# Performance work log

Hardware: AMD Instinct MI355X
Metric: run time of the kernel (lower is better)

Reference implementation:

```python
import jax, jax.numpy as jnp
import numpy as np

B, P = 64, 256          # graphs, nodes per graph
N = B * P
IN, H, C, OUT = 4096, 512, 12, 5
E0 = 131072             # directed edges before symmetrization
EPS = 1e-15


def setup_inputs() -> dict:
    key = jax.random.key(0)
    ks = jax.random.split(key, 12)
    x = jax.random.normal(ks[0], (N, IN), jnp.float32)
    # within-graph random edges, then symmetrize (to_undirected)
    src0 = jax.random.randint(ks[1], (E0,), 0, N)
    off = jax.random.randint(ks[2], (E0,), 0, P)
    dst0 = (src0 // P) * P + off
    edge_index = jnp.stack([jnp.concatenate([src0, dst0]),
                            jnp.concatenate([dst0, src0])])
    batch = jnp.repeat(jnp.arange(B, dtype=jnp.int32), P)
    p = lambda k, sh: 0.02 * jax.random.normal(k, sh, jnp.float32)
    return dict(
        x=x, edge_index=edge_index, batch=batch,
        W1=p(ks[3], (IN, H)), b1=jnp.zeros((H,), jnp.float32),
        Wm1=p(ks[4], (H, H)), bm1=jnp.zeros((H,), jnp.float32),
        Wm2=p(ks[5], (H, C)), bm2=jnp.zeros((C,), jnp.float32),
        Wrel=p(ks[6], (H, H)), brel=jnp.zeros((H,), jnp.float32),
        Wroot=p(ks[7], (H, H)),
        Wl1=p(ks[8], (H, H)), bl1=jnp.zeros((H,), jnp.float32),
        Wl2=p(ks[9], (H, OUT)), bl2=jnp.zeros((OUT,), jnp.float32),
    )


def _forward(x, edge_index, batch, W1, b1, Wm1, bm1, Wm2, bm2,
             Wrel, brel, Wroot, Wl1, bl1, Wl2, bl2):
    src, dst = edge_index[0], edge_index[1]

    # ---- GCNConv(in=4096, out=512): sym-normalized with self-loops ----
    loop = jnp.arange(N)
    src_l = jnp.concatenate([src, loop])
    dst_l = jnp.concatenate([dst, loop])
    deg = jax.ops.segment_sum(jnp.ones_like(src_l, dtype=x.dtype), dst_l,
                              num_segments=N)
    dinv = jnp.where(deg > 0, deg ** -0.5, 0.0)
    norm = dinv[src_l] * dinv[dst_l]
    h = x @ W1                                        # [N,H]
    h = jax.ops.segment_sum(h[src_l] * norm[:, None], dst_l,
                            num_segments=N) + b1
    h = jax.nn.relu(h)

    # ---- to_dense_batch / to_dense_adj (batch is sorted) ----
    counts = jax.ops.segment_sum(jnp.ones((N,), jnp.int32), batch,
                                 num_segments=B)
    starts = jnp.concatenate([jnp.zeros((1,), jnp.int32),
                              jnp.cumsum(counts)[:-1]])
    pos = jnp.arange(N, dtype=jnp.int32) - starts[batch]
    xd = jnp.zeros((B, P, H), h.dtype).at[batch, pos].set(h)   # [B,P,H]
    mask = jnp.zeros((B, P), bool).at[batch, pos].set(True)
    be = batch[src]
    adj = jnp.zeros((B, P, P), h.dtype).at[
        be, src - starts[be], dst - starts[be]].add(1.0)

    # ---- DMoNPooling ----
    maskf = mask.astype(h.dtype)[..., None]            # [B,P,1]
    sel = (xd @ Wm1 + bm1) @ Wm2 + bm2                 # MLP, no act
    sel = jax.nn.softmax(sel, axis=-1)                 # [B,P,C]
    xm = xd * maskf
    sel = sel * maskf
    out = jax.nn.selu(jnp.einsum('bnc,bnh->bch', sel, xm))   # [B,C,H]
    out_adj = jnp.einsum('bnc,bnm,bmk->bck', sel, adj, sel)  # [B,C,C]

    degrees = adj.sum(-1)[..., None] * maskf           # [B,P,1]
    m = degrees.sum((1, 2)) / 2                        # [B]
    ca = jnp.einsum('bnc,bne->bce', sel, degrees)      # [B,C,1]
    cb = jnp.einsum('bne,bnc->bec', degrees, sel)      # [B,1,C]
    normalizer = (ca @ cb) / 2 / m[:, None, None]
    spectral = (-jnp.trace(out_adj - normalizer, axis1=1, axis2=2)
                / 2 / m).mean()

    ss = jnp.einsum('bnc,bnk->bck', sel, sel)
    ss_n = jnp.linalg.norm(ss, axis=(1, 2), keepdims=True)
    eye = jnp.eye(C, dtype=h.dtype)
    sqrtC = jnp.sqrt(jnp.asarray(C, h.dtype))
    ortho = jnp.linalg.norm(ss / ss_n - eye / sqrtC, axis=(1, 2)).mean()

    csize = sel.sum(1)                                 # [B,C]
    cluster = (jnp.linalg.norm(csize, axis=1) / maskf.sum((1, 2))
               * sqrtC - 1).mean()

    # zero diagonal + symmetric degree-normalize coarse adjacency
    out_adj = out_adj * (1.0 - eye)
    d = jnp.sqrt(out_adj.sum(-1))[:, None, :] + EPS    # [B,1,C]
    out_adj = out_adj / d / jnp.swapaxes(d, 1, 2)

    # ---- DenseGraphConv (aggr='add') ----
    h2 = jnp.einsum('bck,bkh->bch', out_adj, out) @ Wrel + brel + out @ Wroot

    g = h2.mean(1)                                     # [B,H]
    g = jax.nn.relu(g @ Wl1 + bl1)
    logits = g @ Wl2 + bl2                             # [B,OUT]
    return logits, cluster + ortho + spectral


def reference(x, edge_index, batch, W1, b1, Wm1, bm1, Wm2, bm2,
              Wrel, brel, Wroot, Wl1, bl1, Wl2, bl2):
    return _forward(x, edge_index, batch, W1, b1, Wm1, bm1, Wm2, bm2,
                    Wrel, brel, Wroot, Wl1, bl1, Wl2, bl2)
```

## Files before the change

kernel.cpp:

```cpp
#include <hip/hip_runtime.h>
#include <stdint.h>

typedef unsigned short u16;
typedef unsigned int   u32;
typedef float  f32x4 __attribute__((ext_vector_type(4)));
typedef u32    u32x2 __attribute__((ext_vector_type(2)));
typedef u32    u32x4 __attribute__((ext_vector_type(4)));
typedef short  s16x8 __attribute__((ext_vector_type(8)));

#define NODES 16384
#define BGR   64
#define PG    256
#define HDIM  512
#define INDIM 4096
#define CCL   12

__device__ __forceinline__ float bf2f(u16 u){ u32 x = ((u32)u) << 16; return __uint_as_float(x); }
__device__ __forceinline__ u16 f2bf(float f){
    u32 x = __float_as_uint(f);
    return (u16)((x + 0x7fffu + ((x >> 16) & 1u)) >> 16);
}
__device__ __forceinline__ u32 pk2(float a, float b){ return (u32)f2bf(a) | ((u32)f2bf(b) << 16); }

__global__ void transpose_bf16(const float* __restrict__ W, u16* __restrict__ Wt, int K, int N){
    __shared__ float tile[32][33];
    int k0 = blockIdx.x * 32, n0 = blockIdx.y * 32;
    int tx = threadIdx.x, ty = threadIdx.y;
    #pragma unroll
    for (int j = 0; j < 4; ++j)
        tile[ty + 8*j][tx] = W[(size_t)(k0 + ty + 8*j) * N + n0 + tx];
    __syncthreads();
    #pragma unroll
    for (int j = 0; j < 4; ++j)
        Wt[(size_t)(n0 + ty + 8*j) * K + k0 + tx] = f2bf(tile[tx][ty + 8*j]);
}

__global__ void transpose_u16(const u16* __restrict__ in, u16* __restrict__ out, int R, int C){
    __shared__ u16 tile[32][33];
    int r0 = blockIdx.x * 32, c0 = blockIdx.y * 32;
    int tx = threadIdx.x, ty = threadIdx.y;
    #pragma unroll
    for (int j = 0; j < 4; ++j)
        tile[ty + 8*j][tx] = in[(size_t)(r0 + ty + 8*j) * C + c0 + tx];
    __syncthreads();
    #pragma unroll
    for (int j = 0; j < 4; ++j)
        out[(size_t)(c0 + ty + 8*j) * R + r0 + tx] = tile[tx][ty + 8*j];
}

__global__ void build_adj(const int* __restrict__ ei, float* __restrict__ adj, int E){
    int e = blockIdx.x * 256 + threadIdx.x;
    if (e < E){
        int s = ei[e];
        int d = ei[E + e];
        atomicAdd(&adj[(size_t)s * 256 + (d & 255)], 1.0f);
    }
}

__global__ void rowsum_deg(const float* __restrict__ adj, float* __restrict__ degs,
                           float* __restrict__ dinv){
    int r = blockIdx.x * 4 + (threadIdx.x >> 6);
    int lane = threadIdx.x & 63;
    const float* row = adj + (size_t)r * 256;
    float s = row[lane] + row[lane + 64] + row[lane + 128] + row[lane + 192];
    #pragma unroll
    for (int m = 1; m < 64; m <<= 1) s += __shfl_xor(s, m);
    if (lane == 0){ degs[r] = s; dinv[r] = 1.0f / sqrtf(s + 1.0f); }
}

template<int AF32, int EPI>
__global__ __launch_bounds__(512, 1) void gemm512(
    const void* __restrict__ Ap, int lda, int abstride,
    const u16* __restrict__ Bt, int ldb, int btstride,
    u16* __restrict__ Out,
    const float* __restrict__ rowscale, const float* __restrict__ bias,
    const u16* __restrict__ aux, int K, int prows)
{
    int m0l = blockIdx.x * 64;
    int g   = blockIdx.y;
    int t = threadIdx.x, lane = t & 63, w = t >> 6;
    int wc = w * 64;
    int grow0 = g * prows + m0l;

    __shared__ __align__(16) u16 a_l[2][64][40];
    __shared__ __align__(16) u16 b_l[2][512][40];

    f32x4 acc[4][4];
    #pragma unroll
    for (int m = 0; m < 4; ++m)
        #pragma unroll
        for (int n = 0; n < 4; ++n) acc[m][n] = (f32x4)0.0f;

    const float* A32 = (const float*)Ap + (size_t)g * abstride;
    const u16*   A16 = (const u16*)Ap + (size_t)g * abstride;
    const u16*   Bp  = Bt + (size_t)g * btstride;

    int arow = t >> 3, acol = (t & 7) * 4;
    int r16 = lane & 15, khalf = (lane >> 4) * 8;
    const int nt = K / 32;

    f32x4 raf0, raf1; u32x2 rah0, rah1; u32x4 rb0[4], rb1[4];

#define LOAD_TILE(S, kt) do {                                                        \
    int k0_ = (kt) * 32;                                                             \
    if (AF32) raf##S = *(const f32x4*)(A32 + (size_t)(m0l + arow) * lda + k0_ + acol);\
    else      rah##S = *(const u32x2*)(A16 + (size_t)(m0l + arow) * lda + k0_ + acol);\
    const u16* bp_ = Bp + (size_t)t * ldb + k0_;                                     \
    _Pragma("unroll")                                                                \
    for (int j_ = 0; j_ < 4; ++j_) rb##S[j_] = *(const u32x4*)(bp_ + j_ * 8);        \
} while (0)

#define STORE_TILE(S, buf) do {                                                      \
    u32x2 aw_;                                                                       \
    if (AF32) { aw_.x = pk2(raf##S.x, raf##S.y); aw_.y = pk2(raf##S.z, raf##S.w); }  \
    else aw_ = rah##S;                                                               \
    *(u32x2*)&a_l[buf][arow][acol] = aw_;                                            \
    _Pragma("unroll")                                                                \
    for (int j_ = 0; j_ < 4; ++j_) *(u32x4*)&b_l[buf][t][j_ * 8] = rb##S[j_];        \
} while (0)

#define COMPUTE(buf) do {                                                            \
    s16x8 af_[4], bf_[4];                                                            \
    _Pragma("unroll")                                                                \
    for (int m_ = 0; m_ < 4; ++m_) af_[m_] = *(const s16x8*)&a_l[buf][m_ * 16 + r16][khalf]; \
    _Pragma("unroll")                                                                \
    for (int n_ = 0; n_ < 4; ++n_) bf_[n_] = *(const s16x8*)&b_l[buf][wc + n_ * 16 + r16][khalf]; \
    _Pragma("unroll")                                                                \
    for (int m_ = 0; m_ < 4; ++m_)                                                   \
        _Pragma("unroll")                                                            \
        for (int n_ = 0; n_ < 4; ++n_)                                               \
            acc[m_][n_] = __builtin_amdgcn_mfma_f32_16x16x32_bf16(af_[m_], bf_[n_], acc[m_][n_], 0, 0, 0); \
} while (0)

    LOAD_TILE(0, 0);
    LOAD_TILE(1, 1);
    STORE_TILE(0, 0);
    __syncthreads();

    for (int i = 0; i < nt; i += 2){
        LOAD_TILE(0, (i + 2 < nt ? i + 2 : nt - 1));
        COMPUTE(0);
        STORE_TILE(1, 1);
        __syncthreads();
        LOAD_TILE(1, (i + 3 < nt ? i + 3 : nt - 1));
        COMPUTE(1);
        STORE_TILE(0, 0);
        __syncthreads();
    }

#undef LOAD_TILE
#undef STORE_TILE
#undef COMPUTE

    int r4 = (lane >> 4) * 4, c16 = lane & 15;
    #pragma unroll
    for (int m = 0; m < 4; ++m)
        #pragma unroll
        for (int n = 0; n < 4; ++n)
            #pragma unroll
            for (int r = 0; r < 4; ++r){
                int gr = grow0 + m * 16 + r4 + r;
                int gc = wc + n * 16 + c16;
                float v = acc[m][n][r];
                if (EPI == 0)      v *= rowscale[gr];
                else if (EPI == 1) v += bias[gc];
                else {
                    v = fmaxf(rowscale[gr] * (v + bf2f(aux[(size_t)gr * 512 + gc])) + bias[gc], 0.f);
                }
                Out[(size_t)gr * 512 + gc] = f2bf(v);
            }
}

__global__ void sel_kernel(const u16* __restrict__ t1, const float* __restrict__ Wm2,
                           const float* __restrict__ bm2, float* __restrict__ sel){
    int n = blockIdx.x * 4 + (threadIdx.x >> 6);
    int lane = threadIdx.x & 63;
    u32x4 v = *(const u32x4*)(t1 + (size_t)n * 512 + lane * 8);
    float tv[8];
    tv[0]=bf2f((u16)(v.x&0xffff)); tv[1]=bf2f((u16)(v.x>>16));
    tv[2]=bf2f((u16)(v.y&0xffff)); tv[3]=bf2f((u16)(v.y>>16));
    tv[4]=bf2f((u16)(v.z&0xffff)); tv[5]=bf2f((u16)(v.z>>16));
    tv[6]=bf2f((u16)(v.w&0xffff)); tv[7]=bf2f((u16)(v.w>>16));
    float acc[CCL];
    #pragma unroll
    for (int c = 0; c < CCL; ++c) acc[c] = 0.f;
    #pragma unroll
    for (int i = 0; i < 8; ++i){
        const float* wr = Wm2 + (size_t)(lane * 8 + i) * CCL;
        #pragma unroll
        for (int c = 0; c < CCL; ++c) acc[c] += tv[i] * wr[c];
    }
    #pragma unroll
    for (int m = 1; m < 64; m <<= 1)
        #pragma unroll
        for (int c = 0; c < CCL; ++c) acc[c] += __shfl_xor(acc[c], m);
    if (lane == 0){
        float mx = -1e30f;
        #pragma unroll
        for (int c = 0; c < CCL; ++c){ acc[c] += bm2[c]; mx = fmaxf(mx, acc[c]); }
        float s = 0.f;
        #pragma unroll
        for (int c = 0; c < CCL; ++c){ acc[c] = expf(acc[c] - mx); s += acc[c]; }
        float inv = 1.f / s;
        #pragma unroll
        for (int c = 0; c < CCL; ++c) sel[(size_t)n * CCL + c] = acc[c] * inv;
    }
}

__device__ __forceinline__ float selu(float x){
    const float sc = 1.0507009873554804934193349852946f;
    const float al = 1.6732632423543772848170429916717f;
    return x > 0.f ? sc * x : sc * al * (expf(x) - 1.f);
}

__global__ void out_kernel(const float* __restrict__ sel, const u16* __restrict__ h1,
                           float* __restrict__ outp){
    int b = blockIdx.x >> 2, hb = blockIdx.x & 3;
    int t = threadIdx.x;
    __shared__ float sel_l[PG * CCL];
    for (int i = t; i < PG * CCL; i += 128) sel_l[i] = sel[(size_t)b * PG * CCL + i];
    __syncthreads();
    int h = hb * 128 + t;
    float acc[CCL];
    #pragma unroll
    for (int c = 0; c < CCL; ++c) acc[c] = 0.f;
    const u16* hp = h1 + (size_t)b * PG * 512 + h;
    for (int n = 0; n < PG; ++n){
        float v = bf2f(hp[(size_t)n * 512]);
        const float* s = sel_l + n * CCL;
        #pragma unroll
        for (int c = 0; c < CCL; ++c) acc[c] += v * s[c];
    }
    #pragma unroll
    for (int c = 0; c < CCL; ++c)
        outp[((size_t)b * CCL + c) * 512 + h] = selu(acc[c]);
}

__global__ void pool_kernel(const float* __restrict__ sel, const float* __restrict__ adj,
                            const float* __restrict__ degs, float* __restrict__ oan,
                            float* __restrict__ scal){
    int b = blockIdx.x, t = threadIdx.x;
    __shared__ float sel_l[PG * CCL];
    __shared__ float u_l[PG * CCL];
    __shared__ float deg_l[PG];
    __shared__ float ss_l[144], oa_l[144];
    __shared__ float ca_l[CCL], cs_l[CCL], rs_l[CCL];
    __shared__ float msum;
    for (int i = t; i < PG * CCL; i += 256) sel_l[i] = sel[(size_t)b * PG * CCL + i];
    deg_l[t] = degs[b * PG + t];
    __syncthreads();
    {
        float u[CCL];
        #pragma unroll
        for (int c = 0; c < CCL; ++c) u[c] = 0.f;
        const float* adjb = adj + (size_t)b * PG * PG;
        for (int j = 0; j < PG; ++j){
            float a = adjb[j * PG + t];
            const float* s = sel_l + j * CCL;
            #pragma unroll
            for (int c = 0; c < CCL; ++c) u[c] += a * s[c];
        }
        #pragma unroll
        for (int c = 0; c < CCL; ++c) u_l[t * CCL + c] = u[c];
    }
    __syncthreads();
    if (t < 144){
        int c = t / 12, k = t % 12;
        float ssv = 0.f, oav = 0.f;
        for (int n = 0; n < PG; ++n){
            ssv += sel_l[n * CCL + c] * sel_l[n * CCL + k];
            oav += sel_l[n * CCL + c] * u_l[n * CCL + k];
        }
        ss_l[t] = ssv; oa_l[t] = oav;
    } else if (t < 156){
        int c = t - 144; float cs = 0.f, ca = 0.f;
        for (int n = 0; n < PG; ++n){
            float s = sel_l[n * CCL + c];
            cs += s; ca += s * deg_l[n];
        }
        cs_l[c] = cs; ca_l[c] = ca;
    } else if (t == 156){
        float s = 0.f;
        for (int n = 0; n < PG; ++n) s += deg_l[n];
        msum = s;
    }
    __syncthreads();
    if (t == 0){
        float m = msum * 0.5f;
        float inv2m = 1.f / (2.f * m);
        float sp = 0.f;
        for (int c = 0; c < CCL; ++c) sp += oa_l[c * 13] - ca_l[c] * ca_l[c] * inv2m;
        scal[b] = -sp * inv2m;
        float s2 = 0.f;
        for (int i = 0; i < 144; ++i) s2 += ss_l[i] * ss_l[i];
        float ssn = sqrtf(s2);
        const float isq = 0.28867513459481288f;
        float o2 = 0.f;
        for (int i = 0; i < 144; ++i){
            float d = ss_l[i] / ssn - ((i % 13 == 0) ? isq : 0.f);
            o2 += d * d;
        }
        scal[64 + b] = sqrtf(o2);
        float c2 = 0.f;
        for (int c = 0; c < CCL; ++c) c2 += cs_l[c] * cs_l[c];
        scal[128 + b] = sqrtf(c2) * (sqrtf(12.f) / 256.f) - 1.f;
    }
    if (t < CCL){
        float r = 0.f;
        for (int k = 0; k < CCL; ++k) if (k != t) r += oa_l[t * CCL + k];
        rs_l[t] = sqrtf(r) + 1e-15f;
    }
    __syncthreads();
    if (t < 144){
        int c = t / 12, k = t % 12;
        float v = (c == k) ? 0.f : oa_l[t] / (rs_l[c] * rs_l[k]);
        oan[(size_t)b * 144 + t] = v;
    }
}

__global__ void head_kernel(const float* __restrict__ outp, const float* __restrict__ oan,
                            const float* __restrict__ Wrel, const float* __restrict__ brel,
                            const float* __restrict__ Wroot,
                            const float* __restrict__ Wl1, const float* __restrict__ bl1,
                            const float* __restrict__ Wl2, const float* __restrict__ bl2,
                            float* __restrict__ dout){
    int b = blockIdx.x, t = threadIdx.x;
    __shared__ float out_l[CCL * 512];
    __shared__ float w12[CCL];
    __shared__ float v1l[512], v2l[512], gprel[512], gl[512];
    for (int i = t; i < CCL * 512; i += 256) out_l[i] = outp[(size_t)b * CCL * 512 + i];
    if (t < CCL){
        float s = 0.f;
        for (int c = 0; c < CCL; ++c) s += oan[(size_t)b * 144 + c * CCL + t];
        w12[t] = s * (1.f / 12.f);
    }
    __syncthreads();
    for (int h = t; h < 512; h += 256){
        float a1 = 0.f, a2 = 0.f;
        #pragma unroll
        for (int k = 0; k < CCL; ++k){ a1 += w12[k] * out_l[k * 512 + h]; a2 += out_l[k * 512 + h]; }
        v1l[h] = a1; v2l[h] = a2 * (1.f / 12.f);
    }
    __syncthreads();
    for (int h = t; h < 512; h += 256){
        float acc = brel[h];
        for (int k = 0; k < 512; ++k)
            acc += v1l[k] * Wrel[(size_t)k * 512 + h] + v2l[k] * Wroot[(size_t)k * 512 + h];
        gprel[h] = acc;
    }
    __syncthreads();
    for (int h = t; h < 512; h += 256){
        float acc = bl1[h];
        for (int k = 0; k < 512; ++k) acc += gprel[k] * Wl1[(size_t)k * 512 + h];
        gl[h] = fmaxf(acc, 0.f);
    }
    __syncthreads();
    if (t < 64){
        float acc[5] = {0.f, 0.f, 0.f, 0.f, 0.f};
        for (int h = t; h < 512; h += 64){
            float g = gl[h];
            #pragma unroll
            for (int o = 0; o < 5; ++o) acc[o] += g * Wl2[(size_t)h * 5 + o];
        }
        #pragma unroll
        for (int m = 1; m < 64; m <<= 1)
            #pragma unroll
            for (int o = 0; o < 5; ++o) acc[o] += __shfl_xor(acc[o], m);
        if (t == 0){
            #pragma unroll
            for (int o = 0; o < 5; ++o) dout[b * 5 + o] = acc[o] + bl2[o];
        }
    }
}

__global__ void loss_kernel(const float* __restrict__ scal, float* __restrict__ dout){
    int t = threadIdx.x;
    float v = scal[t] + scal[64 + t] + scal[128 + t];
    #pragma unroll
    for (int m = 1; m < 64; m <<= 1) v += __shfl_xor(v, m);
    if (t == 0) dout[BGR * 5] = v * (1.f / 64.f);
}

extern "C" void kernel_launch(void* const* d_in, const int* in_sizes, int n_in,
                              void* d_out, int out_size, void* d_ws, size_t ws_size,
                              hipStream_t stream)
{
    const float* x    = (const float*)d_in[0];
    const int*   ei   = (const int*)d_in[1];
    const float* W1   = (const float*)d_in[3];
    const float* b1   = (const float*)d_in[4];
    const float* Wm1  = (const float*)d_in[5];
    const float* bm1  = (const float*)d_in[6];
    const float* Wm2  = (const float*)d_in[7];
    const float* bm2  = (const float*)d_in[8];
    const float* Wrel = (const float*)d_in[9];
    const float* brel = (const float*)d_in[10];
    const float* Wroot= (const float*)d_in[11];
    const float* Wl1  = (const float*)d_in[12];
    const float* bl1  = (const float*)d_in[13];
    const float* Wl2  = (const float*)d_in[14];
    const float* bl2  = (const float*)d_in[15];
    float* dout = (float*)d_out;
    const int E = in_sizes[1] / 2;

    char* w = (char*)d_ws;
    float* adj  = (float*)(w + 0);
    float* degs = (float*)(w + 16777216);
    float* dinv = (float*)(w + 16842752);
    u16*   Wt   = (u16*)  (w + 16908288);
    u16*   Wm1t = (u16*)  (w + 21102592);
    u16*   hs   = (u16*)  (w + 21626880);
    u16*   h1   = (u16*)  (w + 38404096);
    u16*   hsT  = (u16*)  (w + 55181312);
    float* sel  = (float*)(w + 16908288);
    float* outp = (float*)(w + 17694720);
    float* oan  = (float*)(w + 19267584);
    float* scal = (float*)(w + 19304448);
    u16* t1 = hs;

    hipMemsetAsync(adj, 0, 16777216, stream);

    hipLaunchKernelGGL(transpose_bf16, dim3(INDIM / 32, HDIM / 32), dim3(32, 8), 0, stream,
                       W1, Wt, INDIM, HDIM);
    hipLaunchKernelGGL(transpose_bf16, dim3(HDIM / 32, HDIM / 32), dim3(32, 8), 0, stream,
                       Wm1, Wm1t, HDIM, HDIM);
    hipLaunchKernelGGL(build_adj, dim3((E + 255) / 256), dim3(256), 0, stream, ei, adj, E);
    hipLaunchKernelGGL(rowsum_deg, dim3(NODES / 4), dim3(256), 0, stream, adj, degs, dinv);

    hipLaunchKernelGGL((gemm512<1, 0>), dim3(NODES / 64, 1), dim3(512), 0, stream,
                       (const void*)x, INDIM, 0, Wt, INDIM, 0, hs,
                       dinv, (const float*)nullptr, (const u16*)nullptr, INDIM, 0);

    hipLaunchKernelGGL(transpose_u16, dim3(NODES / 32, HDIM / 32), dim3(32, 8), 0, stream,
                       hs, hsT, NODES, HDIM);

    hipLaunchKernelGGL((gemm512<1, 2>), dim3(PG / 64, BGR), dim3(512), 0, stream,
                       (const void*)adj, PG, PG * PG, hsT, NODES, PG, h1,
                       dinv, b1, hs, PG, PG);

    hipLaunchKernelGGL((gemm512<0, 1>), dim3(NODES / 64, 1), dim3(512), 0, stream,
                       (const void*)h1, HDIM, 0, Wm1t, HDIM, 0, t1,
                       (const float*)nullptr, bm1, (const u16*)nullptr, HDIM, 0);

    hipLaunchKernelGGL(sel_kernel, dim3(NODES / 4), dim3(256), 0, stream, t1, Wm2, bm2, sel);
    hipLaunchKernelGGL(out_kernel, dim3(BGR * 4), dim3(128), 0, stream, sel, h1, outp);
    hipLaunchKernelGGL(pool_kernel, dim3(BGR), dim3(256), 0, stream, sel, adj, degs, oan, scal);
    hipLaunchKernelGGL(head_kernel, dim3(BGR), dim3(256), 0, stream, outp, oan,
                       Wrel, brel, Wroot, Wl1, bl1, Wl2, bl2, dout);
    hipLaunchKernelGGL(loss_kernel, dim3(1), dim3(64), 0, stream, scal, dout);
}
```

Measured before the change: 866.2 us.

## Split-K the input GEMM, tile N in the MLP GEMM, and parallelize head across blocks

The GEMM kernel is templated on warps per block and split-K. The large x@W1 GEMM now splits K in two and writes bf16 partials, and a new combine kernel sums them and applies dinv. The Wm1 GEMM uses 256-wide N tiles with twice as many blocks to raise occupancy. The per-graph head kernel, which ran serial 512x512 matvecs, is replaced by a pooling kernel plus batched head GEMV kernels that spread work over 256 blocks, and out_kernel handles two columns per thread. The cost is extra partial-buffer traffic, bf16 rounding of the partials, and more kernel launches.

```diff
diff --git a/kernel.cpp b/kernel.cpp
--- a/kernel.cpp
+++ b/kernel.cpp
@@ -3,6 +3,7 @@
 
 typedef unsigned short u16;
 typedef unsigned int   u32;
+typedef float  f32x2 __attribute__((ext_vector_type(2)));
 typedef float  f32x4 __attribute__((ext_vector_type(4)));
 typedef u32    u32x2 __attribute__((ext_vector_type(2)));
 typedef u32    u32x4 __attribute__((ext_vector_type(4)));
@@ -68,22 +69,28 @@
     if (lane == 0){ degs[r] = s; dinv[r] = 1.0f / sqrtf(s + 1.0f); }
 }
 
-template<int AF32, int EPI>
-__global__ __launch_bounds__(512, 1) void gemm512(
-    const void* __restrict__ Ap, int lda, int abstride,
-    const u16* __restrict__ Bt, int ldb, int btstride,
-    u16* __restrict__ Out,
+template<int AF32, int EPI, int NT, int SK>
+__global__ __launch_bounds__(NT*64, NT == 8 ? 4 : 3) void gemm512(
+    const void* __restrict__ Ap, int lda, long abstride,
+    const u16* __restrict__ Bt, int ldb, long btstride,
+    u16* __restrict__ Out, size_t osplit,
     const float* __restrict__ rowscale, const float* __restrict__ bias,
-    const u16* __restrict__ aux, int K, int prows)
+    const u16* __restrict__ aux, int K, int prows, int nbn)
 {
-    int m0l = blockIdx.x * 64;
-    int g   = blockIdx.y;
+    constexpr int BN  = NT * 64;
+    constexpr int AEL = 2048 / BN;
+    int bx = blockIdx.x;
+    int s    = bx % SK;  bx /= SK;
+    int nblk = bx % nbn;
+    int m0l  = (bx / nbn) * 64;
+    int n0   = nblk * BN;
+    int g    = blockIdx.y;
     int t = threadIdx.x, lane = t & 63, w = t >> 6;
     int wc = w * 64;
     int grow0 = g * prows + m0l;
 
-    __shared__ __align__(16) u16 a_l[2][64][40];
-    __shared__ __align__(16) u16 b_l[2][512][40];
+    __shared__ __align__(16) u16 a_l[2][64][36];
+    __shared__ __align__(16) u16 b_l[2][BN][34];
 
     f32x4 acc[4][4];
     #pragma unroll
@@ -95,40 +102,57 @@
     const u16*   A16 = (const u16*)Ap + (size_t)g * abstride;
     const u16*   Bp  = Bt + (size_t)g * btstride;
 
-    int arow = t >> 3, acol = (t & 7) * 4;
+    int arow, acol;
+    if (NT == 8){ arow = t >> 3; acol = (t & 7) * 4; }
+    else        { arow = t >> 2; acol = (t & 3) * 8; }
     int r16 = lane & 15, khalf = (lane >> 4) * 8;
-    const int nt = K / 32;
-
-    f32x4 raf0, raf1; u32x2 rah0, rah1; u32x4 rb0[4], rb1[4];
-
-#define LOAD_TILE(S, kt) do {                                                        \
-    int k0_ = (kt) * 32;                                                             \
-    if (AF32) raf##S = *(const f32x4*)(A32 + (size_t)(m0l + arow) * lda + k0_ + acol);\
-    else      rah##S = *(const u32x2*)(A16 + (size_t)(m0l + arow) * lda + k0_ + acol);\
-    const u16* bp_ = Bp + (size_t)t * ldb + k0_;                                     \
-    _Pragma("unroll")                                                                \
-    for (int j_ = 0; j_ < 4; ++j_) rb##S[j_] = *(const u32x4*)(bp_ + j_ * 8);        \
+    const int kbase = s * (K / SK);
+    const int nt = (K / SK) / 32;
+
+    f32x4 raF[2][AEL / 4];
+    u32   raH[2][AEL / 2];
+    u32x4 rb[2][4];
+
+#define LOAD_TILE(S, kt) do {                                                         \
+    int k0_ = kbase + (kt) * 32;                                                      \
+    if (AF32){                                                                        \
+        _Pragma("unroll")                                                             \
+        for (int q_ = 0; q_ < AEL / 4; ++q_)                                          \
+            raF[S][q_] = *(const f32x4*)(A32 + (size_t)(m0l + arow) * lda + k0_ + acol + q_ * 4); \
+    } else {                                                                          \
+        if (AEL == 4) *(u32x2*)&raH[S][0] = *(const u32x2*)(A16 + (size_t)(m0l + arow) * lda + k0_ + acol); \
+        else          *(u32x4*)&raH[S][0] = *(const u32x4*)(A16 + (size_t)(m0l + arow) * lda + k0_ + acol); \
+    }                                                                                 \
+    const u16* bp_ = Bp + (size_t)(n0 + t) * ldb + k0_;                               \
+    _Pragma("unroll")                                                                 \
+    for (int j_ = 0; j_ < 4; ++j_) rb[S][j_] = *(const u32x4*)(bp_ + j_ * 8);         \
 } while (0)
 
-#define STORE_TILE(S, buf) do {                                                      \
-    u32x2 aw_;                                                                       \
-    if (AF32) { aw_.x = pk2(raf##S.x, raf##S.y); aw_.y = pk2(raf##S.z, raf##S.w); }  \
-    else aw_ = rah##S;                                                               \
-    *(u32x2*)&a_l[buf][arow][acol] = aw_;                                            \
-    _Pragma("unroll")                                                                \
-    for (int j_ = 0; j_ < 4; ++j_) *(u32x4*)&b_l[buf][t][j_ * 8] = rb##S[j_];        \
+#define STORE_TILE(S, buf) do {                                                       \
+    if (AF32){                                                                        \
+        _Pragma("unroll")                                                             \
+        for (int q_ = 0; q_ < AEL / 4; ++q_){                                         \
+            u32x2 aw_ = { pk2(raF[S][q_].x, raF[S][q_].y), pk2(raF[S][q_].z, raF[S][q_].w) }; \
+            *(u32x2*)&a_l[buf][arow][acol + q_ * 4] = aw_;                            \
+        }                                                                             \
+    } else {                                                                          \
+        if (AEL == 4) *(u32x2*)&a_l[buf][arow][acol] = *(u32x2*)&raH[S][0];           \
+        else          *(u32x4*)&a_l[buf][arow][acol] = *(u32x4*)&raH[S][0];           \
+    }                                                                                 \
+    _Pragma("unroll")                                                                 \
+    for (int j_ = 0; j_ < 4; ++j_) *(u32x4*)&b_l[buf][t][j_ * 8] = rb[S][j_];         \
 } while (0)
 
-#define COMPUTE(buf) do {                                                            \
-    s16x8 af_[4], bf_[4];                                                            \
-    _Pragma("unroll")                                                                \
+#define COMPUTE(buf) do {                                                             \
+    s16x8 af_[4], bf_[4];                                                             \
+    _Pragma("unroll")                                                                 \
     for (int m_ = 0; m_ < 4; ++m_) af_[m_] = *(const s16x8*)&a_l[buf][m_ * 16 + r16][khalf]; \
-    _Pragma("unroll")                                                                \
+    _Pragma("unroll")                                                                 \
     for (int n_ = 0; n_ < 4; ++n_) bf_[n_] = *(const s16x8*)&b_l[buf][wc + n_ * 16 + r16][khalf]; \
-    _Pragma("unroll")                                                                \
-    for (int m_ = 0; m_ < 4; ++m_)                                                   \
-        _Pragma("unroll")                                                            \
-        for (int n_ = 0; n_ < 4; ++n_)                                               \
+    _Pragma("unroll")                                                                 \
+    for (int m_ = 0; m_ < 4; ++m_)                                                    \
+        _Pragma("unroll")                                                             \
+        for (int n_ = 0; n_ < 4; ++n_)                                                \
             acc[m_][n_] = __builtin_amdgcn_mfma_f32_16x16x32_bf16(af_[m_], bf_[n_], acc[m_][n_], 0, 0, 0); \
 } while (0)
 
@@ -152,6 +176,7 @@
 #undef STORE_TILE
 #undef COMPUTE
 
+    u16* Op = Out + (size_t)s * osplit;
     int r4 = (lane >> 4) * 4, c16 = lane & 15;
     #pragma unroll
     for (int m = 0; m < 4; ++m)
@@ -160,15 +185,32 @@
             #pragma unroll
             for (int r = 0; r < 4; ++r){
                 int gr = grow0 + m * 16 + r4 + r;
-                int gc = wc + n * 16 + c16;
+                int gc = n0 + wc + n * 16 + c16;
                 float v = acc[m][n][r];
                 if (EPI == 0)      v *= rowscale[gr];
                 else if (EPI == 1) v += bias[gc];
-                else {
+                else if (EPI == 2)
                     v = fmaxf(rowscale[gr] * (v + bf2f(aux[(size_t)gr * 512 + gc])) + bias[gc], 0.f);
-                }
-                Out[(size_t)gr * 512 + gc] = f2bf(v);
+                Op[(size_t)gr * 512 + gc] = f2bf(v);
             }
+}
+
+__global__ void combine_k(const u16* __restrict__ p, const float* __restrict__ dinv,
+                          u16* __restrict__ hs){
+    size_t i = (size_t)blockIdx.x * 256 + threadIdx.x;
+    u32x4 a = *(const u32x4*)(p + i * 8);
+    u32x4 b = *(const u32x4*)(p + (size_t)NODES * 512 + i * 8);
+    float d = dinv[i >> 6];
+    u32x4 o;
+    o.x = pk2(d * (bf2f((u16)(a.x & 0xffff)) + bf2f((u16)(b.x & 0xffff))),
+              d * (bf2f((u16)(a.x >> 16))    + bf2f((u16)(b.x >> 16))));
+    o.y = pk2(d * (bf2f((u16)(a.y & 0xffff)) + bf2f((u16)(b.y & 0xffff))),
+              d * (bf2f((u16)(a.y >> 16))    + bf2f((u16)(b.y >> 16))));
+    o.z = pk2(d * (bf2f((u16)(a.z & 0xffff)) + bf2f((u16)(b.z & 0xffff))),
+              d * (bf2f((u16)(a.z >> 16))    + bf2f((u16)(b.z >> 16))));
+    o.w = pk2(d * (bf2f((u16)(a.w & 0xffff)) + bf2f((u16)(b.w & 0xffff))),
+              d * (bf2f((u16)(a.w >> 16))    + bf2f((u16)(b.w >> 16))));
+    *(u32x4*)(hs + i * 8) = o;
 }
 
 __global__ void sel_kernel(const u16* __restrict__ t1, const float* __restrict__ Wm2,
@@ -215,25 +257,28 @@
 
 __global__ void out_kernel(const float* __restrict__ sel, const u16* __restrict__ h1,
                            float* __restrict__ outp){
-    int b = blockIdx.x >> 2, hb = blockIdx.x & 3;
+    int b = blockIdx.x >> 1, hb = blockIdx.x & 1;
     int t = threadIdx.x;
     __shared__ float sel_l[PG * CCL];
     for (int i = t; i < PG * CCL; i += 128) sel_l[i] = sel[(size_t)b * PG * CCL + i];
     __syncthreads();
-    int h = hb * 128 + t;
-    float acc[CCL];
-    #pragma unroll
-    for (int c = 0; c < CCL; ++c) acc[c] = 0.f;
-    const u16* hp = h1 + (size_t)b * PG * 512 + h;
+    int h0 = hb * 256 + t * 2;
+    float acc0[CCL], acc1[CCL];
+    #pragma unroll
+    for (int c = 0; c < CCL; ++c){ acc0[c] = 0.f; acc1[c] = 0.f; }
+    const u16* hp = h1 + (size_t)b * PG * 512 + h0;
     for (int n = 0; n < PG; ++n){
-        float v = bf2f(hp[(size_t)n * 512]);
+        u32 hv = *(const u32*)(hp + (size_t)n * 512);
+        float v0 = bf2f((u16)(hv & 0xffff)), v1 = bf2f((u16)(hv >> 16));
         const float* s = sel_l + n * CCL;
         #pragma unroll
-        for (int c = 0; c < CCL; ++c) acc[c] += v * s[c];
-    }
-    #pragma unroll
-    for (int c = 0; c < CCL; ++c)
-        outp[((size_t)b * CCL + c) * 512 + h] = selu(acc[c]);
+        for (int c = 0; c < CCL; ++c){ acc0[c] += v0 * s[c]; acc1[c] += v1 * s[c]; }
+    }
+    #pragma unroll
+    for (int c = 0; c < CCL; ++c){
+        f32x2 ov = { selu(acc0[c]), selu(acc1[c]) };
+        *(f32x2*)&outp[((size_t)b * CCL + c) * 512 + h0] = ov;
+    }
 }
 
 __global__ void pool_kernel(const float* __restrict__ sel, const float* __restrict__ adj,
@@ -318,16 +363,11 @@
     }
 }
 
-__global__ void head_kernel(const float* __restrict__ outp, const float* __restrict__ oan,
-                            const float* __restrict__ Wrel, const float* __restrict__ brel,
-                            const float* __restrict__ Wroot,
-                            const float* __restrict__ Wl1, const float* __restrict__ bl1,
-                            const float* __restrict__ Wl2, const float* __restrict__ bl2,
-                            float* __restrict__ dout){
+__global__ void pool2_kernel(const float* __restrict__ outp, const float* __restrict__ oan,
+                             float* __restrict__ v1T, float* __restrict__ v2T){
     int b = blockIdx.x, t = threadIdx.x;
     __shared__ float out_l[CCL * 512];
     __shared__ float w12[CCL];
-    __shared__ float v1l[512], v2l[512], gprel[512], gl[512];
     for (int i = t; i < CCL * 512; i += 256) out_l[i] = outp[(size_t)b * CCL * 512 + i];
     if (t < CCL){
         float s = 0.f;
@@ -335,42 +375,52 @@
         w12[t] = s * (1.f / 12.f);
     }
     __syncthreads();
-    for (int h = t; h < 512; h += 256){
+    #pragma unroll
+    for (int q = 0; q < 2; ++q){
+        int h = t + q * 256;
         float a1 = 0.f, a2 = 0.f;
         #pragma unroll
-        for (int k = 0; k < CCL; ++k){ a1 += w12[k] * out_l[k * 512 + h]; a2 += out_l[k * 512 + h]; }
-        v1l[h] = a1; v2l[h] = a2 * (1.f / 12.f);
-    }
-    __syncthreads();
-    for (int h = t; h < 512; h += 256){
-        float acc = brel[h];
-        for (int k = 0; k < 512; ++k)
-            acc += v1l[k] * Wrel[(size_t)k * 512 + h] + v2l[k] * Wroot[(size_t)k * 512 + h];
-        gprel[h] = acc;
-    }
-    __syncthreads();
-    for (int h = t; h < 512; h += 256){
-        float acc = bl1[h];
-        for (int k = 0; k < 512; ++k) acc += gprel[k] * Wl1[(size_t)k * 512 + h];
-        gl[h] = fmaxf(acc, 0.f);
-    }
-    __syncthreads();
-    if (t < 64){
-        float acc[5] = {0.f, 0.f, 0.f, 0.f, 0.f};
-        for (int h = t; h < 512; h += 64){
-            float g = gl[h];
-            #pragma unroll
-            for (int o = 0; o < 5; ++o) acc[o] += g * Wl2[(size_t)h * 5 + o];
+        for (int k = 0; k < CCL; ++k){
+            float o = out_l[k * 512 + h];
+            a1 += w12[k] * o; a2 += o;
         }
-        #pragma unroll
-        for (int m = 1; m < 64; m <<= 1)
-            #pragma unroll
-            for (int o = 0; o < 5; ++o) acc[o] += __shfl_xor(acc[o], m);
-        if (t == 0){
-            #pragma unroll
-            for (int o = 0; o < 5; ++o) dout[b * 5 + o] = acc[o] + bl2[o];
-        }
-    }
+        v1T[(size_t)h * 64 + b] = a1;
+        v2T[(size_t)h * 64 + b] = a2 * (1.f / 12.f);
+    }
+}
+
+template<int TWO, int RELU>
+__global__ void head_ab(const float* __restrict__ V1T, const float* __restrict__ W1,
+                        const float* __restrict__ V2T, const float* __restrict__ W2,
+                        const float* __restrict__ bias, float* __restrict__ OT){
+    int c0 = blockIdx.x * 2;
+    int t = threadIdx.x;
+    int g = t & 63, hc = (t >> 6) & 1, ks = t >> 7;
+    __shared__ float red[2][2][64];
+    float acc = 0.f;
+    int kend = ks * 256 + 256;
+    for (int k = ks * 256; k < kend; ++k){
+        acc += V1T[(size_t)k * 64 + g] * W1[(size_t)k * 512 + c0 + hc];
+        if (TWO) acc += V2T[(size_t)k * 64 + g] * W2[(size_t)k * 512 + c0 + hc];
+    }
+    red[hc][ks][g] = acc;
+    __syncthreads();
+    if (t < 128){
+        int hc2 = t >> 6, g2 = t & 63;
+        float v = red[hc2][0][g2] + red[hc2][1][g2] + bias[c0 + hc2];
+        if (RELU) v = fmaxf(v, 0.f);
+        OT[(size_t)(c0 + hc2) * 64 + g2] = v;
+    }
+}
+
+__global__ void head_c(const float* __restrict__ glT, const float* __restrict__ Wl2,
+                       const float* __restrict__ bl2, float* __restrict__ dout){
+    int t = threadIdx.x;
+    int o = t >> 6, g = t & 63;
+    float acc = 0.f;
+    for (int k = 0; k < 512; ++k)
+        acc += glT[(size_t)k * 64 + g] * Wl2[(size_t)k * 5 + o];
+    dout[g * 5 + o] = acc + bl2[o];
 }
 
 __global__ void loss_kernel(const float* __restrict__ scal, float* __restrict__ dout){
@@ -412,11 +462,16 @@
     u16*   hs   = (u16*)  (w + 21626880);
     u16*   h1   = (u16*)  (w + 38404096);
     u16*   hsT  = (u16*)  (w + 55181312);
+    float* v1T  = (float*)(w + 71958528);
+    float* v2T  = (float*)(w + 72089600);
+    float* gpT  = (float*)(w + 72220672);
+    float* glT  = (float*)(w + 72351744);
     float* sel  = (float*)(w + 16908288);
     float* outp = (float*)(w + 17694720);
     float* oan  = (float*)(w + 19267584);
     float* scal = (float*)(w + 19304448);
     u16* t1 = hs;
+    u16* parts = h1;
 
     hipMemsetAsync(adj, 0, 16777216, stream);
 
@@ -427,25 +482,32 @@
     hipLaunchKernelGGL(build_adj, dim3((E + 255) / 256), dim3(256), 0, stream, ei, adj, E);
     hipLaunchKernelGGL(rowsum_deg, dim3(NODES / 4), dim3(256), 0, stream, adj, degs, dinv);
 
-    hipLaunchKernelGGL((gemm512<1, 0>), dim3(NODES / 64, 1), dim3(512), 0, stream,
-                       (const void*)x, INDIM, 0, Wt, INDIM, 0, hs,
-                       dinv, (const float*)nullptr, (const u16*)nullptr, INDIM, 0);
+    hipLaunchKernelGGL((gemm512<1, 3, 8, 2>), dim3((NODES / 64) * 2, 1), dim3(512), 0, stream,
+                       (const void*)x, INDIM, 0L, Wt, INDIM, 0L, parts, (size_t)NODES * 512,
+                       (const float*)nullptr, (const float*)nullptr, (const u16*)nullptr,
+                       INDIM, 0, 1);
+    hipLaunchKernelGGL(combine_k, dim3(NODES * 512 / 2048), dim3(256), 0, stream,
+                       parts, dinv, hs);
 
     hipLaunchKernelGGL(transpose_u16, dim3(NODES / 32, HDIM / 32), dim3(32, 8), 0, stream,
                        hs, hsT, NODES, HDIM);
 
-    hipLaunchKernelGGL((gemm512<1, 2>), dim3(PG / 64, BGR), dim3(512), 0, stream,
-                       (const void*)adj, PG, PG * PG, hsT, NODES, PG, h1,
-                       dinv, b1, hs, PG, PG);
-
-    hipLaunchKernelGGL((gemm512<0, 1>), dim3(NODES / 64, 1), dim3(512), 0, stream,
-                       (const void*)h1, HDIM, 0, Wm1t, HDIM, 0, t1,
-                       (const float*)nullptr, bm1, (const u16*)nullptr, HDIM, 0);
+    hipLaunchKernelGGL((gemm512<1, 2, 8, 1>), dim3(PG / 64, BGR), dim3(512), 0, stream,
+                       (const void*)adj, PG, (long)PG * PG, hsT, NODES, (long)PG, h1, (size_t)0,
+                       dinv, b1, hs, PG, PG, 1);
+
+    hipLaunchKernelGGL((gemm512<0, 1, 4, 1>), dim3((NODES / 64) * 2, 1), dim3(256), 0, stream,
+                       (const void*)h1, HDIM, 0L, Wm1t, HDIM, 0L, t1, (size_t)0,
+                       (const float*)nullptr, bm1, (const u16*)nullptr, HDIM, 0, 2);
 
     hipLaunchKernelGGL(sel_kernel, dim3(NODES / 4), dim3(256), 0, stream, t1, Wm2, bm2, sel);
-    hipLaunchKernelGGL(out_kernel, dim3(BGR * 4), dim3(128), 0, stream, sel, h1, outp);
+    hipLaunchKernelGGL(out_kernel, dim3(BGR * 2), dim3(128), 0, stream, sel, h1, outp);
     hipLaunchKernelGGL(pool_kernel, dim3(BGR), dim3(256), 0, stream, sel, adj, degs, oan, scal);
-    hipLaunchKernelGGL(head_kernel, dim3(BGR), dim3(256), 0, stream, outp, oan,
-                       Wrel, brel, Wroot, Wl1, bl1, Wl2, bl2, dout);
+    hipLaunchKernelGGL(pool2_kernel, dim3(BGR), dim3(256), 0, stream, outp, oan, v1T, v2T);
+    hipLaunchKernelGGL((head_ab<1, 0>), dim3(256), dim3(256), 0, stream,
+                       v1T, Wrel, v2T, Wroot, brel, gpT);
+    hipLaunchKernelGGL((head_ab<0, 1>), dim3(256), dim3(256), 0, stream,
+                       gpT, Wl1, (const float*)nullptr, (const float*)nullptr, bl1, glT);
+    hipLaunchKernelGGL(head_c, dim3(1), dim3(320), 0, stream, glT, Wl2, bl2, dout);
     hipLaunchKernelGGL(loss_kernel, dim3(1), dim3(64), 0, stream, scal, dout);
 }
```

Measured after the change: 839.8 us. -3.0%, faster.
